# Kernel optimization log

Measured on AMD Instinct MI355X. Metric: run time of the kernel, lower is better.

## Reference

```python
import jax, jax.numpy as jnp
import numpy as np

DIM = 96; HEADS = 3; DHEAD = 32; GSS = 4; PATCH = 32; B = 128; G = 8
INNER = HEADS * DHEAD  # == DIM
SCALE = DHEAD ** -0.5
EPS = 1e-5


def _rbf(x):
    # FastKAN RBF basis on grid [-2, 2] with G centers -> (..., G)
    centers = jnp.linspace(-2.0, 2.0, G)
    h = 4.0 / (G - 1)
    return jnp.exp(-(((x[..., None] - centers) / h) ** 2))


def _kan_pointwise(x, wb, ws):
    # Pointwise KAN conv: (b, Cin, *spatial) -> (b, Cout, *spatial)
    # y = W_base @ silu(x) + W_spline @ rbf(x)
    b, cin = x.shape[0], x.shape[1]
    sp = x.shape[2:]
    xs = x.reshape(b, cin, -1)                       # (b, Cin, L)
    y = jnp.einsum('oi,bil->bol', wb, jax.nn.silu(xs))
    y = y + jnp.einsum('oig,bilg->bol', ws, _rbf(xs))
    return y.reshape(b, wb.shape[0], *sp)


def setup_inputs() -> dict:
    key = jax.random.key(0)
    ks = jax.random.split(key, 8)
    inp = {
        'x': jax.random.normal(ks[0], (B, DIM, PATCH, PATCH), jnp.float32),
        'group_tokens': jax.random.normal(ks[1], (DIM,), jnp.float32),
        'qkv_wb': jax.random.normal(ks[2], (3 * DIM, DIM), jnp.float32) * (DIM ** -0.5),
        'qkv_ws': jax.random.normal(ks[3], (3 * DIM, DIM, G), jnp.float32) * 0.02,
        'ln_g': jnp.ones((DHEAD,), jnp.float32),
        'ln_b': jnp.zeros((DHEAD,), jnp.float32),
        'gt_wb': jax.random.normal(ks[4], (2 * INNER, INNER), jnp.float32) * (INNER ** -0.5),
        'gt_ws': jax.random.normal(ks[5], (2 * INNER, INNER, G), jnp.float32) * 0.02,
        'out_wb': jax.random.normal(ks[6], (DIM, INNER), jnp.float32) * (INNER ** -0.5),
        'out_ws': jax.random.normal(ks[7], (DIM, INNER, G), jnp.float32) * 0.02,
    }
    return inp


def reference(x, group_tokens, qkv_wb, qkv_ws, ln_g, ln_b, gt_wb, gt_ws, out_wb, out_ws):
    b, c, H, W = x.shape
    g = GSS
    nx, ny = H // g, W // g
    nw = nx * ny                                    # number of windows
    bp = b * nw
    n = g * g + 1                                   # window tokens incl. group token

    # b c (h g1) (w g2) -> (b h w) c (g1 g2)
    xw = x.reshape(b, c, nx, g, ny, g).transpose(0, 2, 4, 1, 3, 5).reshape(bp, c, g * g)
    tok = jnp.broadcast_to(group_tokens[None, :, None], (bp, c, 1))
    xw = jnp.concatenate([tok, xw], axis=-1)        # (bp, c, n)

    qkv = _kan_pointwise(xw, qkv_wb, qkv_ws)        # (bp, 3c, n)
    q, k, v = jnp.split(qkv, 3, axis=1)

    def split_heads(t):  # b (h d) n -> b h n d
        return t.reshape(bp, HEADS, DHEAD, n).transpose(0, 1, 3, 2)

    q, k, v = map(split_heads, (q, k, v))
    q = q * SCALE
    # channel-attention within window: contract over token axis n
    dots = jnp.einsum('bhni,bhnj->bhij', q, k)      # (bp, h, d, d)
    attn = jax.nn.softmax(dots, axis=-1)
    out = jnp.einsum('bhij,bhnj->bhni', attn, v)    # (bp, h, n, d)

    gt = out[:, :, 0]                               # (bp, h, d) group tokens
    gf = out[:, :, 1:]                              # (bp, h, g*g, d)
    gt = gt.reshape(b, nw, HEADS, DHEAD).transpose(0, 2, 1, 3)            # (b, h, nw, d)
    gf = gf.reshape(b, nw, HEADS, g * g, DHEAD).transpose(0, 2, 1, 3, 4)  # (b, h, nw, gg, d)

    # group_tokens_to_qk: LN(d) -> GELU -> KAN conv over nw (channels h*d -> 2*h*d)
    mu = gt.mean(-1, keepdims=True)
    var = ((gt - mu) ** 2).mean(-1, keepdims=True)
    h_ = (gt - mu) * jax.lax.rsqrt(var + EPS) * ln_g + ln_b
    h_ = jax.nn.gelu(h_, approximate=False)
    hh = h_.transpose(0, 1, 3, 2).reshape(b, HEADS * DHEAD, nw)           # b (h c) n
    qk = _kan_pointwise(hh, gt_wb, gt_ws)                                 # (b, 2*h*d, nw)
    qk = qk.reshape(b, HEADS, 2 * DHEAD, nw).transpose(0, 1, 3, 2)        # (b, h, nw, 2d)
    w_q, w_k = jnp.split(qk, 2, axis=-1)
    w_q = w_q * SCALE
    w_attn = jax.nn.softmax(jnp.einsum('bhid,bhjd->bhij', w_q, w_k), axis=-1)
    agg = jnp.einsum('bhij,bhjwd->bhiwd', w_attn, gf)                     # (b, h, nw, gg, d)

    # b h (x y) (g1 g2) d -> b (h d) (x g1) (y g2)
    fmap = agg.reshape(b, HEADS, nx, ny, g, g, DHEAD)
    fmap = fmap.transpose(0, 1, 6, 2, 4, 3, 5).reshape(b, HEADS * DHEAD, H, W)

    return _kan_pointwise(fmap, out_wb, out_ws)     # (b, dim, H, W)
```

## Files before the change

kernel.cpp:

```cpp
#include <hip/hip_runtime.h>
#include <cstddef>

#define SCALE 0.17677669529663687f
#define EPS 1e-5f

typedef __attribute__((ext_vector_type(8))) __bf16 bf16x8;
typedef __attribute__((ext_vector_type(16))) float f32x16;
typedef __attribute__((ext_vector_type(8))) unsigned short ushort8;

__device__ __forceinline__ unsigned short f2bf(float f) {
    unsigned u = __float_as_uint(f);
    return (unsigned short)((u + 0x7fffu + ((u >> 16) & 1u)) >> 16);
}
__device__ __forceinline__ float bf2f(unsigned short h) {
    return __uint_as_float(((unsigned)h) << 16);
}
__device__ __forceinline__ unsigned cvt_pk_bf16(float a, float b) {
    unsigned r;
    asm("v_cvt_pk_bf16_f32 %0, %1, %2" : "=v"(r) : "v"(a), "v"(b));
    return r;
}

#define MFMA32(a, b, c) __builtin_amdgcn_mfma_f32_32x32x16_bf16(a, b, c, 0, 0, 0)

#define GLD_LDS16(gsrc, ldst) \
    __builtin_amdgcn_global_load_lds((const __attribute__((address_space(1))) void*)(gsrc), \
                                     (__attribute__((address_space(3))) void*)(ldst), 16, 0, 0)

__global__ __launch_bounds__(256)
void prep_frag32(const float* __restrict__ wb, const float* __restrict__ ws,
                 unsigned short* __restrict__ Wf, int MTT)
{
    int idx = blockIdx.x * 256 + threadIdx.x;
    int total = 27 * MTT * 4 * 64;
    if (idx >= total) return;
    int lane = idx & 63;
    int t = idx >> 6;
    int hl = t & 1, kf = (t >> 1) & 1;
    int mt = (t >> 2) % MTT, s = (t >> 2) / MTT;
    int cg = s / 9, f = s - cg * 9;
    int m = mt * 32 + (lane & 31);
    int kg = lane >> 5;
    ushort8 v;
    #pragma unroll
    for (int j = 0; j < 8; ++j) {
        int c = cg * 32 + kf * 16 + kg * 8 + j;
        float w = (f == 0) ? wb[m * 96 + c] : ws[(m * 96 + c) * 8 + (f - 1)];
        unsigned short hi = f2bf(w);
        v[j] = hl ? f2bf(w - bf2f(hi)) : hi;
    }
    *reinterpret_cast<ushort8*>(Wf + (size_t)t * 512 + lane * 8) = v;
}

template<int MTT, int MODE>
__global__ __launch_bounds__(256, 4)
void kan_mfma(const float* __restrict__ xin, const float* __restrict__ token,
              const unsigned short* __restrict__ Wf, float* __restrict__ out)
{
    __shared__ __align__(16) char smem[40960];
    char* sA = smem;
    char* sB = smem + 24576;

    const int tid = threadIdx.x, lane = tid & 63, wid = tid >> 6;

    int n0, mb;
    if (MODE == 0) {
        int xcd = blockIdx.x & 7, idx = blockIdx.x >> 3;
        int nloc = idx / 3; mb = idx - nloc * 3;
        n0 = (xcd * 136 + nloc) * 128;
    } else if (MODE == 1) {
        int xcd = blockIdx.x & 7;
        n0 = (xcd * 128 + (blockIdx.x >> 3)) * 128; mb = 0;
    } else {
        mb = blockIdx.x & 1; n0 = (blockIdx.x >> 1) * 128;
    }

    auto issueA = [&](int s, int buf) {
        #pragma unroll
        for (int c0 = 0; c0 < 3; ++c0) {
            int c = wid + c0 * 4;
            const unsigned short* src = Wf + ((size_t)s * MTT * 4 + mb * 12 + c) * 512 + lane * 8;
            GLD_LDS16(src, sA + (buf * 12 + c) * 1024);
        }
    };
    issueA(0, 0);

    const int ct = tid & 127, kgp = tid >> 7;
    const int lane_in = kgp * 32 + (ct & 31);
    const int p = n0 + ct;
    const float* gbase;
    int gstride;
    if (MODE == 0) {
        int w = p / 17, l = p - w * 17;
        if (l == 0) { gbase = token; gstride = 1; }
        else {
            int b = w >> 6, wl = w & 63;
            int wx = wl >> 3, wy = wl & 7;
            int jj = l - 1, gx = jj >> 2, gy = jj & 3;
            gbase = xin + (size_t)b * 98304 + (wx * 4 + gx) * 32 + wy * 4 + gy;
            gstride = 1024;
        }
    } else if (MODE == 1) {
        gbase = xin + (size_t)(p >> 10) * 98304 + (p & 1023);
        gstride = 1024;
    } else {
        gbase = xin + (size_t)(p >> 6) * 6144 + (p & 63);
        gstride = 64;
    }

    f32x16 acc[3];
    #pragma unroll
    for (int mt = 0; mt < 3; ++mt)
        #pragma unroll
        for (int r = 0; r < 16; ++r) acc[mt][r] = 0.f;

    float rr[16], du[16];

    auto phiInit = [&](int cg, char* d0, char* d1) {
        float ph[16];
        #pragma unroll
        for (int t = 0; t < 2; ++t)
            #pragma unroll
            for (int j = 0; j < 8; ++j) {
                int q = t * 8 + j;
                float xv = gbase[(size_t)(cg * 32 + t * 16 + kgp * 8 + j) * gstride];
                ph[q] = __fdividef(xv, 1.f + __expf(-xv));
                float a = fmaf(xv, 1.75f, 3.5f);
                rr[q] = __expf(-a * a);
                du[q] = __expf(fminf(fmaf(a, 2.f, -1.f), 80.f));
            }
        uint4 w0, w1;
        w0.x = cvt_pk_bf16(ph[0], ph[1]);  w0.y = cvt_pk_bf16(ph[2], ph[3]);
        w0.z = cvt_pk_bf16(ph[4], ph[5]);  w0.w = cvt_pk_bf16(ph[6], ph[7]);
        w1.x = cvt_pk_bf16(ph[8], ph[9]);  w1.y = cvt_pk_bf16(ph[10], ph[11]);
        w1.z = cvt_pk_bf16(ph[12], ph[13]); w1.w = cvt_pk_bf16(ph[14], ph[15]);
        *reinterpret_cast<uint4*>(d0) = w0;
        *reinterpret_cast<uint4*>(d1) = w1;
    };
    auto phiRbf = [&](bool upd, char* d0, char* d1) {
        if (upd) {
            #pragma unroll
            for (int q = 0; q < 16; ++q) { rr[q] *= du[q]; du[q] *= 0.1353352832366127f; }
        }
        uint4 w0, w1;
        w0.x = cvt_pk_bf16(rr[0], rr[1]);  w0.y = cvt_pk_bf16(rr[2], rr[3]);
        w0.z = cvt_pk_bf16(rr[4], rr[5]);  w0.w = cvt_pk_bf16(rr[6], rr[7]);
        w1.x = cvt_pk_bf16(rr[8], rr[9]);  w1.y = cvt_pk_bf16(rr[10], rr[11]);
        w1.z = cvt_pk_bf16(rr[12], rr[13]); w1.w = cvt_pk_bf16(rr[14], rr[15]);
        *reinterpret_cast<uint4*>(d0) = w0;
        *reinterpret_cast<uint4*>(d1) = w1;
    };

    phiInit(0, sB + (ct >> 5) * 1024 + lane_in * 16,
               sB + (4 + (ct >> 5)) * 1024 + lane_in * 16);

    #pragma unroll
    for (int s = 0; s < 27; ++s) {
        int sb = s & 1;
        __syncthreads();
        if (s + 1 < 27) issueA(s + 1, (s + 1) & 1);
        {
            const char* Ab = sA + sb * 12288;
            const char* Bb = sB + sb * 8192;
            bf16x8 b0 = *reinterpret_cast<const bf16x8*>(Bb + wid * 1024 + lane * 16);
            bf16x8 b1 = *reinterpret_cast<const bf16x8*>(Bb + (4 + wid) * 1024 + lane * 16);
            #pragma unroll
            for (int mt = 0; mt < 3; ++mt) {
                const char* fb = Ab + mt * 4096 + lane * 16;
                bf16x8 a0 = *reinterpret_cast<const bf16x8*>(fb);
                bf16x8 a1 = *reinterpret_cast<const bf16x8*>(fb + 1024);
                bf16x8 a2 = *reinterpret_cast<const bf16x8*>(fb + 2048);
                bf16x8 a3 = *reinterpret_cast<const bf16x8*>(fb + 3072);
                acc[mt] = MFMA32(a0, b0, acc[mt]);
                acc[mt] = MFMA32(a1, b0, acc[mt]);
                acc[mt] = MFMA32(a2, b1, acc[mt]);
                acc[mt] = MFMA32(a3, b1, acc[mt]);
            }
        }
        if (s + 1 < 27) {
            char* d0 = sB + ((s + 1) & 1) * 8192 + (ct >> 5) * 1024 + lane_in * 16;
            int fn = (s + 1) % 9;
            if (fn == 0) phiInit((s + 1) / 9, d0, d0 + 4096);
            else phiRbf(fn != 1, d0, d0 + 4096);
        }
    }

    if (MODE == 0) {
        float* T = reinterpret_cast<float*>(smem);
        const int cw = wid * 32 + (lane & 31);
        const int c2 = tid & 127, q = tid >> 7;
        const int pp = n0 + c2, w = pp / 17, l = pp - w * 17;
        float* dst = out + (size_t)w * 4896 + l * 288 + mb * 96 + q * 16;
        #pragma unroll
        for (int mt = 0; mt < 3; ++mt) {
            __syncthreads();
            #pragma unroll
            for (int r = 0; r < 16; ++r) {
                int row = (r & 3) + 8 * (r >> 2) + 4 * (lane >> 5);
                T[cw * 33 + row] = acc[mt][r];
            }
            __syncthreads();
            const float* srcT = T + c2 * 33 + q * 16;
            #pragma unroll
            for (int jj = 0; jj < 4; ++jj) {
                float4 v;
                v.x = srcT[jj * 4 + 0]; v.y = srcT[jj * 4 + 1];
                v.z = srcT[jj * 4 + 2]; v.w = srcT[jj * 4 + 3];
                reinterpret_cast<float4*>(dst + mt * 32)[jj] = v;
            }
        }
    } else {
        const int colL = n0 + wid * 32 + (lane & 31);
        #pragma unroll
        for (int mt = 0; mt < 3; ++mt) {
            #pragma unroll
            for (int r = 0; r < 16; ++r) {
                int row = mb * 96 + mt * 32 + (r & 3) + 8 * (r >> 2) + 4 * (lane >> 5);
                float v = acc[mt][r];
                if (MODE == 1)
                    out[(size_t)(colL >> 10) * 98304 + (size_t)row * 1024 + (colL & 1023)] = v;
                else
                    out[(size_t)row * 8192 + colL] = v;
            }
        }
    }
}

__global__ __launch_bounds__(256)
void attn1(const float* __restrict__ qkv, float* __restrict__ gt, float* __restrict__ gf)
{
    __shared__ float sw[17][288];
    __shared__ float sa[3][32][33];
    const int w = blockIdx.x, tid = threadIdx.x;

    const float4* src = reinterpret_cast<const float4*>(qkv + (size_t)w * 4896);
    float4* dstl = reinterpret_cast<float4*>(&sw[0][0]);
    for (int e = tid; e < 1224; e += 256) dstl[e] = src[e];
    __syncthreads();

    for (int e = tid; e < 3072; e += 256) {
        int h = e >> 10, r = e & 1023, i = r >> 5, j = r & 31;
        float s = 0.f;
        #pragma unroll
        for (int l = 0; l < 17; ++l) s += sw[l][h * 32 + i] * sw[l][96 + h * 32 + j];
        sa[h][i][j] = s * SCALE;
    }
    __syncthreads();
    if (tid < 96) {
        int h = tid >> 5, i = tid & 31;
        float m = -1e30f;
        for (int j = 0; j < 32; ++j) m = fmaxf(m, sa[h][i][j]);
        float sum = 0.f;
        for (int j = 0; j < 32; ++j) { float e_ = __expf(sa[h][i][j] - m); sa[h][i][j] = e_; sum += e_; }
        float inv = 1.f / sum;
        for (int j = 0; j < 32; ++j) sa[h][i][j] *= inv;
    }
    __syncthreads();
    const int b = w >> 6, wl = w & 63;
    for (int e = tid; e < 1632; e += 256) {
        int h = e / 544, r = e - h * 544, l = r >> 5, i = r & 31;
        float s = 0.f;
        #pragma unroll
        for (int j = 0; j < 32; ++j) s += sa[h][i][j] * sw[l][192 + h * 32 + j];
        if (l == 0) gt[(((size_t)b * 3 + h) * 64 + wl) * 32 + i] = s;
        else        gf[((((size_t)b * 3 + h) * 64 + wl) * 16 + (l - 1)) * 32 + i] = s;
    }
}

__global__ __launch_bounds__(256)
void ln_gelu(const float* __restrict__ gt, const float* __restrict__ lng,
             const float* __restrict__ lnb, float* __restrict__ hh)
{
    int row = blockIdx.x * 8 + (threadIdx.x >> 5);
    int d = threadIdx.x & 31;
    float x = gt[(size_t)row * 32 + d];
    float s = x, s2 = x * x;
    #pragma unroll
    for (int m = 16; m >= 1; m >>= 1) { s += __shfl_xor(s, m, 32); s2 += __shfl_xor(s2, m, 32); }
    float mu = s * (1.f / 32.f);
    float var = s2 * (1.f / 32.f) - mu * mu;
    float h = (x - mu) * rsqrtf(var + EPS) * lng[d] + lnb[d];
    float g = 0.5f * h * (1.f + erff(h * 0.70710678118654752f));
    int b = row / 192, r = row - b * 192;
    int hd = r >> 6, wl = r & 63;
    hh[((size_t)b * 96 + hd * 32 + d) * 64 + wl] = g;
}

__global__ __launch_bounds__(256)
void attn2a(const float* __restrict__ qk, float* __restrict__ wattn)
{
    int bh = blockIdx.x;
    int b = bh / 3, h = bh - b * 3;
    __shared__ float swq[64][33];
    __shared__ float swk[64][33];
    __shared__ float sd[64][65];
    int tid = threadIdx.x;
    for (int e = tid; e < 2048; e += 256) {
        int d = e >> 6, i = e & 63;
        swq[i][d] = qk[((size_t)h * 64 + d) * 8192 + b * 64 + i] * SCALE;
        swk[i][d] = qk[((size_t)h * 64 + 32 + d) * 8192 + b * 64 + i];
    }
    __syncthreads();
    for (int e = tid; e < 4096; e += 256) {
        int i = e >> 6, j = e & 63;
        float s = 0.f;
        #pragma unroll
        for (int d = 0; d < 32; ++d) s += swq[i][d] * swk[j][d];
        sd[i][j] = s;
    }
    __syncthreads();
    if (tid < 64) {
        float m = -1e30f;
        for (int j = 0; j < 64; ++j) m = fmaxf(m, sd[tid][j]);
        float sum = 0.f;
        for (int j = 0; j < 64; ++j) { float e_ = __expf(sd[tid][j] - m); sd[tid][j] = e_; sum += e_; }
        float inv = 1.f / sum;
        for (int j = 0; j < 64; ++j) sd[tid][j] *= inv;
    }
    __syncthreads();
    for (int e = tid; e < 4096; e += 256)
        wattn[(size_t)bh * 4096 + e] = sd[e >> 6][e & 63];
}

__global__ __launch_bounds__(256)
void attn2b(const float* __restrict__ wattn, const float* __restrict__ gf,
            float* __restrict__ fmap)
{
    int blk = blockIdx.x;
    int ct = blk & 3, bh = blk >> 2;
    int b = bh / 3, h = bh - b * 3;
    __shared__ float sa[64][65];
    __shared__ float sg[64][129];
    int tid = threadIdx.x;
    for (int e = tid; e < 4096; e += 256) sa[e >> 6][e & 63] = wattn[(size_t)bh * 4096 + e];
    for (int e = tid; e < 8192; e += 256) {
        int j = e >> 7, c = e & 127;
        sg[j][c] = gf[((size_t)bh * 64 + j) * 512 + ct * 128 + c];
    }
    __syncthreads();
    int txc = tid & 31, tyi = tid >> 5;
    float acc[8][4];
    #pragma unroll
    for (int ii = 0; ii < 8; ++ii)
        #pragma unroll
        for (int c = 0; c < 4; ++c) acc[ii][c] = 0.f;
    for (int j = 0; j < 64; ++j) {
        float g0[4];
        #pragma unroll
        for (int c = 0; c < 4; ++c) g0[c] = sg[j][txc + c * 32];
        #pragma unroll
        for (int ii = 0; ii < 8; ++ii) {
            float a = sa[tyi + ii * 8][j];
            #pragma unroll
            for (int c = 0; c < 4; ++c) acc[ii][c] += a * g0[c];
        }
    }
    __syncthreads();
    #pragma unroll
    for (int ii = 0; ii < 8; ++ii)
        #pragma unroll
        for (int c = 0; c < 4; ++c)
            sg[tyi + ii * 8][txc + c * 32] = acc[ii][c];
    __syncthreads();
    for (int e = tid; e < 8192; e += 256) {
        int d = e >> 8;
        int nx = (e >> 5) & 7;
        int cp = e & 31;
        int ny = cp >> 2, gy = cp & 3;
        float v = sg[nx * 8 + ny][gy * 32 + d];
        fmap[(((size_t)b * 96 + h * 32 + d) * 32 + nx * 4 + ct) * 32 + cp] = v;
    }
}

extern "C" void kernel_launch(void* const* d_in, const int* in_sizes, int n_in,
                              void* d_out, int out_size, void* d_ws, size_t ws_size,
                              hipStream_t stream)
{
    const float* x      = (const float*)d_in[0];
    const float* tok    = (const float*)d_in[1];
    const float* qkv_wb = (const float*)d_in[2];
    const float* qkv_ws = (const float*)d_in[3];
    const float* lng    = (const float*)d_in[4];
    const float* lnb    = (const float*)d_in[5];
    const float* gt_wb  = (const float*)d_in[6];
    const float* gt_ws  = (const float*)d_in[7];
    const float* out_wb = (const float*)d_in[8];
    const float* out_ws = (const float*)d_in[9];
    float* out = (float*)d_out;
    float* ws  = (float*)d_ws;

    const size_t OFF_QKV   = 0;
    const size_t OFF_FMAP  = 0;
    const size_t OFF_WATTN = 12582912;
    const size_t OFF_WF2   = 40108032;
    const size_t OFF_GT    = OFF_WF2 + 165888;
    const size_t OFF_GF    = OFF_GT + 786432;
    const size_t OFF_HH    = OFF_GF + 12582912;
    const size_t OFF_QK    = OFF_HH + 786432;
    const size_t OFF_WF1   = OFF_QK + 1572864;
    const size_t OFF_WF3   = OFF_WF1 + 248832;
    const size_t TOTAL     = OFF_WF3 + 82944;
    if (ws_size < TOTAL * sizeof(float)) return;

    unsigned short* wf1 = (unsigned short*)(ws + OFF_WF1);
    unsigned short* wf2 = (unsigned short*)(ws + OFF_WF2);
    unsigned short* wf3 = (unsigned short*)(ws + OFF_WF3);

    prep_frag32<<<243, 256, 0, stream>>>(qkv_wb, qkv_ws, wf1, 9);
    prep_frag32<<<162, 256, 0, stream>>>(gt_wb,  gt_ws,  wf2, 6);
    prep_frag32<<< 81, 256, 0, stream>>>(out_wb, out_ws, wf3, 3);

    kan_mfma<9, 0><<<3264, 256, 0, stream>>>(x, tok, wf1, ws + OFF_QKV);
    attn1<<<8192, 256, 0, stream>>>(ws + OFF_QKV, ws + OFF_GT, ws + OFF_GF);
    ln_gelu<<<3072, 256, 0, stream>>>(ws + OFF_GT, lng, lnb, ws + OFF_HH);
    kan_mfma<6, 2><<<128, 256, 0, stream>>>(ws + OFF_HH, nullptr, wf2, ws + OFF_QK);
    attn2a<<<384, 256, 0, stream>>>(ws + OFF_QK, ws + OFF_WATTN);
    attn2b<<<1536, 256, 0, stream>>>(ws + OFF_WATTN, ws + OFF_GF, ws + OFF_FMAP);
    kan_mfma<3, 1><<<1024, 256, 0, stream>>>(ws + OFF_FMAP, nullptr, wf3, out);
}
```

Measured before the change: 446.5 us.

## Keep activation fragments in registers and double the KAN GEMM N-tile

Restructures the KAN MFMA kernel so the activation basis values (silu and RBF) stay in registers as MFMA operands instead of being staged through shared memory. Each wave now covers 64 columns, so one block handles 256 points and the grid shrinks by half. The operand roles are swapped, which changes the accumulator layout: the QKV and QK outputs are now written directly in point-major order without an LDS transpose, and attn2a is changed to read QK in the new layout. This removes the shared-memory B traffic and barriers tied to it, at the cost of twice the accumulator registers, lower occupancy (launch bounds 2) and less coalesced direct stores.

```diff
diff --git a/kernel.cpp b/kernel.cpp
--- a/kernel.cpp
+++ b/kernel.cpp
@@ -53,26 +53,25 @@
 }
 
 template<int MTT, int MODE>
-__global__ __launch_bounds__(256, 4)
+__global__ __launch_bounds__(256, 2)
 void kan_mfma(const float* __restrict__ xin, const float* __restrict__ token,
               const unsigned short* __restrict__ Wf, float* __restrict__ out)
 {
-    __shared__ __align__(16) char smem[40960];
-    char* sA = smem;
-    char* sB = smem + 24576;
+    __shared__ __align__(16) char smem[2 * 12 * 1024];
 
     const int tid = threadIdx.x, lane = tid & 63, wid = tid >> 6;
+    const int kg = lane >> 5, cl = lane & 31;
 
     int n0, mb;
     if (MODE == 0) {
         int xcd = blockIdx.x & 7, idx = blockIdx.x >> 3;
         int nloc = idx / 3; mb = idx - nloc * 3;
-        n0 = (xcd * 136 + nloc) * 128;
+        n0 = (xcd * 68 + nloc) * 256;
     } else if (MODE == 1) {
         int xcd = blockIdx.x & 7;
-        n0 = (xcd * 128 + (blockIdx.x >> 3)) * 128; mb = 0;
+        n0 = (xcd * 64 + (blockIdx.x >> 3)) * 256; mb = 0;
     } else {
-        mb = blockIdx.x & 1; n0 = (blockIdx.x >> 1) * 128;
+        mb = blockIdx.x & 1; n0 = (blockIdx.x >> 1) * 256;
     }
 
     auto issueA = [&](int s, int buf) {
@@ -80,149 +79,170 @@
         for (int c0 = 0; c0 < 3; ++c0) {
             int c = wid + c0 * 4;
             const unsigned short* src = Wf + ((size_t)s * MTT * 4 + mb * 12 + c) * 512 + lane * 8;
-            GLD_LDS16(src, sA + (buf * 12 + c) * 1024);
+            GLD_LDS16(src, smem + (buf * 12 + c) * 1024);
         }
     };
     issueA(0, 0);
 
-    const int ct = tid & 127, kgp = tid >> 7;
-    const int lane_in = kgp * 32 + (ct & 31);
-    const int p = n0 + ct;
-    const float* gbase;
-    int gstride;
-    if (MODE == 0) {
-        int w = p / 17, l = p - w * 17;
-        if (l == 0) { gbase = token; gstride = 1; }
-        else {
-            int b = w >> 6, wl = w & 63;
-            int wx = wl >> 3, wy = wl & 7;
-            int jj = l - 1, gx = jj >> 2, gy = jj & 3;
-            gbase = xin + (size_t)b * 98304 + (wx * 4 + gx) * 32 + wy * 4 + gy;
-            gstride = 1024;
-        }
-    } else if (MODE == 1) {
-        gbase = xin + (size_t)(p >> 10) * 98304 + (p & 1023);
-        gstride = 1024;
-    } else {
-        gbase = xin + (size_t)(p >> 6) * 6144 + (p & 63);
-        gstride = 64;
-    }
-
-    f32x16 acc[3];
-    #pragma unroll
-    for (int mt = 0; mt < 3; ++mt)
-        #pragma unroll
-        for (int r = 0; r < 16; ++r) acc[mt][r] = 0.f;
-
-    float rr[16], du[16];
-
-    auto phiInit = [&](int cg, char* d0, char* d1) {
-        float ph[16];
-        #pragma unroll
-        for (int t = 0; t < 2; ++t)
-            #pragma unroll
-            for (int j = 0; j < 8; ++j) {
-                int q = t * 8 + j;
-                float xv = gbase[(size_t)(cg * 32 + t * 16 + kgp * 8 + j) * gstride];
-                ph[q] = __fdividef(xv, 1.f + __expf(-xv));
-                float a = fmaf(xv, 1.75f, 3.5f);
-                rr[q] = __expf(-a * a);
-                du[q] = __expf(fminf(fmaf(a, 2.f, -1.f), 80.f));
-            }
-        uint4 w0, w1;
-        w0.x = cvt_pk_bf16(ph[0], ph[1]);  w0.y = cvt_pk_bf16(ph[2], ph[3]);
-        w0.z = cvt_pk_bf16(ph[4], ph[5]);  w0.w = cvt_pk_bf16(ph[6], ph[7]);
-        w1.x = cvt_pk_bf16(ph[8], ph[9]);  w1.y = cvt_pk_bf16(ph[10], ph[11]);
-        w1.z = cvt_pk_bf16(ph[12], ph[13]); w1.w = cvt_pk_bf16(ph[14], ph[15]);
-        *reinterpret_cast<uint4*>(d0) = w0;
-        *reinterpret_cast<uint4*>(d1) = w1;
+    const float* gbv[2];
+    int gsv[2];
+    #pragma unroll
+    for (int nt = 0; nt < 2; ++nt) {
+        int p = n0 + wid * 64 + nt * 32 + cl;
+        if (MODE == 0) {
+            int w = p / 17, l = p - w * 17;
+            if (l == 0) { gbv[nt] = token; gsv[nt] = 1; }
+            else {
+                int b = w >> 6, wl = w & 63;
+                int wx = wl >> 3, wy = wl & 7;
+                int jj = l - 1, gx = jj >> 2, gy = jj & 3;
+                gbv[nt] = xin + (size_t)b * 98304 + (wx * 4 + gx) * 32 + wy * 4 + gy;
+                gsv[nt] = 1024;
+            }
+        } else if (MODE == 1) {
+            gbv[nt] = xin + (size_t)(p >> 10) * 98304 + (p & 1023);
+            gsv[nt] = 1024;
+        } else {
+            gbv[nt] = xin + (size_t)(p >> 6) * 6144 + (p & 63);
+            gsv[nt] = 64;
+        }
+    }
+
+    f32x16 acc[2][3];
+    #pragma unroll
+    for (int nt = 0; nt < 2; ++nt)
+        #pragma unroll
+        for (int mt = 0; mt < 3; ++mt)
+            #pragma unroll
+            for (int r = 0; r < 16; ++r) acc[nt][mt][r] = 0.f;
+
+    float rr[2][16], du[2][16];
+    bf16x8 pk[2][2];
+
+    auto phiInit = [&](int cg) {
+        #pragma unroll
+        for (int nt = 0; nt < 2; ++nt) {
+            float ph[16];
+            #pragma unroll
+            for (int t = 0; t < 2; ++t)
+                #pragma unroll
+                for (int j = 0; j < 8; ++j) {
+                    int q = t * 8 + j;
+                    float xv = gbv[nt][(size_t)(cg * 32 + t * 16 + kg * 8 + j) * gsv[nt]];
+                    ph[q] = __fdividef(xv, 1.f + __expf(-xv));
+                    float a = fmaf(xv, 1.75f, 3.5f);
+                    rr[nt][q] = __expf(-a * a);
+                    du[nt][q] = __expf(fminf(fmaf(a, 2.f, -1.f), 80.f));
+                }
+            #pragma unroll
+            for (int t = 0; t < 2; ++t) {
+                uint4 w;
+                w.x = cvt_pk_bf16(ph[t * 8 + 0], ph[t * 8 + 1]);
+                w.y = cvt_pk_bf16(ph[t * 8 + 2], ph[t * 8 + 3]);
+                w.z = cvt_pk_bf16(ph[t * 8 + 4], ph[t * 8 + 5]);
+                w.w = cvt_pk_bf16(ph[t * 8 + 6], ph[t * 8 + 7]);
+                pk[nt][t] = *reinterpret_cast<bf16x8*>(&w);
+            }
+        }
     };
-    auto phiRbf = [&](bool upd, char* d0, char* d1) {
-        if (upd) {
-            #pragma unroll
-            for (int q = 0; q < 16; ++q) { rr[q] *= du[q]; du[q] *= 0.1353352832366127f; }
-        }
-        uint4 w0, w1;
-        w0.x = cvt_pk_bf16(rr[0], rr[1]);  w0.y = cvt_pk_bf16(rr[2], rr[3]);
-        w0.z = cvt_pk_bf16(rr[4], rr[5]);  w0.w = cvt_pk_bf16(rr[6], rr[7]);
-        w1.x = cvt_pk_bf16(rr[8], rr[9]);  w1.y = cvt_pk_bf16(rr[10], rr[11]);
-        w1.z = cvt_pk_bf16(rr[12], rr[13]); w1.w = cvt_pk_bf16(rr[14], rr[15]);
-        *reinterpret_cast<uint4*>(d0) = w0;
-        *reinterpret_cast<uint4*>(d1) = w1;
+    auto phiRbf = [&](bool upd) {
+        #pragma unroll
+        for (int nt = 0; nt < 2; ++nt) {
+            if (upd) {
+                #pragma unroll
+                for (int q = 0; q < 16; ++q) { rr[nt][q] *= du[nt][q]; du[nt][q] *= 0.1353352832366127f; }
+            }
+            #pragma unroll
+            for (int t = 0; t < 2; ++t) {
+                uint4 w;
+                w.x = cvt_pk_bf16(rr[nt][t * 8 + 0], rr[nt][t * 8 + 1]);
+                w.y = cvt_pk_bf16(rr[nt][t * 8 + 2], rr[nt][t * 8 + 3]);
+                w.z = cvt_pk_bf16(rr[nt][t * 8 + 4], rr[nt][t * 8 + 5]);
+                w.w = cvt_pk_bf16(rr[nt][t * 8 + 6], rr[nt][t * 8 + 7]);
+                pk[nt][t] = *reinterpret_cast<bf16x8*>(&w);
+            }
+        }
     };
 
-    phiInit(0, sB + (ct >> 5) * 1024 + lane_in * 16,
-               sB + (4 + (ct >> 5)) * 1024 + lane_in * 16);
-
     #pragma unroll
     for (int s = 0; s < 27; ++s) {
-        int sb = s & 1;
         __syncthreads();
         if (s + 1 < 27) issueA(s + 1, (s + 1) & 1);
-        {
-            const char* Ab = sA + sb * 12288;
-            const char* Bb = sB + sb * 8192;
-            bf16x8 b0 = *reinterpret_cast<const bf16x8*>(Bb + wid * 1024 + lane * 16);
-            bf16x8 b1 = *reinterpret_cast<const bf16x8*>(Bb + (4 + wid) * 1024 + lane * 16);
-            #pragma unroll
-            for (int mt = 0; mt < 3; ++mt) {
-                const char* fb = Ab + mt * 4096 + lane * 16;
-                bf16x8 a0 = *reinterpret_cast<const bf16x8*>(fb);
-                bf16x8 a1 = *reinterpret_cast<const bf16x8*>(fb + 1024);
-                bf16x8 a2 = *reinterpret_cast<const bf16x8*>(fb + 2048);
-                bf16x8 a3 = *reinterpret_cast<const bf16x8*>(fb + 3072);
-                acc[mt] = MFMA32(a0, b0, acc[mt]);
-                acc[mt] = MFMA32(a1, b0, acc[mt]);
-                acc[mt] = MFMA32(a2, b1, acc[mt]);
-                acc[mt] = MFMA32(a3, b1, acc[mt]);
-            }
-        }
-        if (s + 1 < 27) {
-            char* d0 = sB + ((s + 1) & 1) * 8192 + (ct >> 5) * 1024 + lane_in * 16;
-            int fn = (s + 1) % 9;
-            if (fn == 0) phiInit((s + 1) / 9, d0, d0 + 4096);
-            else phiRbf(fn != 1, d0, d0 + 4096);
+        const int fn = s % 9;
+        if (fn == 0) phiInit(s / 9);
+        else phiRbf(fn != 1);
+
+        const char* Ab = smem + (s & 1) * 12288;
+        #pragma unroll
+        for (int mt = 0; mt < 3; ++mt) {
+            const char* fb = Ab + mt * 4096 + lane * 16;
+            bf16x8 b0h = *reinterpret_cast<const bf16x8*>(fb);
+            bf16x8 b0l = *reinterpret_cast<const bf16x8*>(fb + 1024);
+            bf16x8 b1h = *reinterpret_cast<const bf16x8*>(fb + 2048);
+            bf16x8 b1l = *reinterpret_cast<const bf16x8*>(fb + 3072);
+            #pragma unroll
+            for (int nt = 0; nt < 2; ++nt) {
+                acc[nt][mt] = MFMA32(pk[nt][0], b0h, acc[nt][mt]);
+                acc[nt][mt] = MFMA32(pk[nt][0], b0l, acc[nt][mt]);
+                acc[nt][mt] = MFMA32(pk[nt][1], b1h, acc[nt][mt]);
+                acc[nt][mt] = MFMA32(pk[nt][1], b1l, acc[nt][mt]);
+            }
         }
     }
 
     if (MODE == 0) {
+        #pragma unroll
+        for (int nt = 0; nt < 2; ++nt)
+            #pragma unroll
+            for (int r = 0; r < 16; ++r) {
+                int p = n0 + wid * 64 + nt * 32 + (r & 3) + 8 * (r >> 2) + 4 * kg;
+                int w = p / 17, l = p - w * 17;
+                float* dst = out + (size_t)w * 4896 + l * 288 + mb * 96 + cl;
+                dst[0]  = acc[nt][0][r];
+                dst[32] = acc[nt][1][r];
+                dst[64] = acc[nt][2][r];
+            }
+    } else if (MODE == 2) {
+        #pragma unroll
+        for (int nt = 0; nt < 2; ++nt)
+            #pragma unroll
+            for (int r = 0; r < 16; ++r) {
+                int p = n0 + wid * 64 + nt * 32 + (r & 3) + 8 * (r >> 2) + 4 * kg;
+                float* dst = out + (size_t)p * 192 + mb * 96 + cl;
+                dst[0]  = acc[nt][0][r];
+                dst[32] = acc[nt][1][r];
+                dst[64] = acc[nt][2][r];
+            }
+    } else {
         float* T = reinterpret_cast<float*>(smem);
-        const int cw = wid * 32 + (lane & 31);
-        const int c2 = tid & 127, q = tid >> 7;
-        const int pp = n0 + c2, w = pp / 17, l = pp - w * 17;
-        float* dst = out + (size_t)w * 4896 + l * 288 + mb * 96 + q * 16;
-        #pragma unroll
-        for (int mt = 0; mt < 3; ++mt) {
-            __syncthreads();
-            #pragma unroll
-            for (int r = 0; r < 16; ++r) {
-                int row = (r & 3) + 8 * (r >> 2) + 4 * (lane >> 5);
-                T[cw * 33 + row] = acc[mt][r];
-            }
-            __syncthreads();
-            const float* srcT = T + c2 * 33 + q * 16;
-            #pragma unroll
-            for (int jj = 0; jj < 4; ++jj) {
-                float4 v;
-                v.x = srcT[jj * 4 + 0]; v.y = srcT[jj * 4 + 1];
-                v.z = srcT[jj * 4 + 2]; v.w = srcT[jj * 4 + 3];
-                reinterpret_cast<float4*>(dst + mt * 32)[jj] = v;
-            }
-        }
-    } else {
-        const int colL = n0 + wid * 32 + (lane & 31);
-        #pragma unroll
-        for (int mt = 0; mt < 3; ++mt) {
-            #pragma unroll
-            for (int r = 0; r < 16; ++r) {
-                int row = mb * 96 + mt * 32 + (r & 3) + 8 * (r >> 2) + 4 * (lane >> 5);
-                float v = acc[mt][r];
-                if (MODE == 1)
-                    out[(size_t)(colL >> 10) * 98304 + (size_t)row * 1024 + (colL & 1023)] = v;
-                else
-                    out[(size_t)row * 8192 + colL] = v;
-            }
-        }
+        #pragma unroll
+        for (int mt = 0; mt < 3; ++mt)
+            #pragma unroll
+            for (int ch = 0; ch < 2; ++ch) {
+                __syncthreads();
+                if ((wid >> 1) == ch) {
+                    #pragma unroll
+                    for (int nt = 0; nt < 2; ++nt)
+                        #pragma unroll
+                        for (int r = 0; r < 16; ++r) {
+                            int pl = (wid & 1) * 64 + nt * 32 + (r & 3) + 8 * (r >> 2) + 4 * kg;
+                            T[cl * 129 + pl] = acc[nt][mt][r];
+                        }
+                }
+                __syncthreads();
+                int m = tid >> 3, p0 = (tid & 7) * 16;
+                int col = n0 + ch * 128 + p0;
+                const float* rowT = T + m * 129 + p0;
+                float* dst = out + (size_t)(col >> 10) * 98304
+                           + (size_t)(mb * 96 + mt * 32 + m) * 1024 + (col & 1023);
+                #pragma unroll
+                for (int j = 0; j < 16; j += 4) {
+                    float4 v;
+                    v.x = rowT[j + 0]; v.y = rowT[j + 1];
+                    v.z = rowT[j + 2]; v.w = rowT[j + 3];
+                    *reinterpret_cast<float4*>(dst + j) = v;
+                }
+            }
     }
 }
 
@@ -296,9 +316,10 @@
     __shared__ float sd[64][65];
     int tid = threadIdx.x;
     for (int e = tid; e < 2048; e += 256) {
-        int d = e >> 6, i = e & 63;
-        swq[i][d] = qk[((size_t)h * 64 + d) * 8192 + b * 64 + i] * SCALE;
-        swk[i][d] = qk[((size_t)h * 64 + 32 + d) * 8192 + b * 64 + i];
+        int i = e >> 5, d = e & 31;
+        const float* row = qk + ((size_t)b * 64 + i) * 192 + h * 64;
+        swq[i][d] = row[d] * SCALE;
+        swk[i][d] = row[32 + d];
     }
     __syncthreads();
     for (int e = tid; e < 4096; e += 256) {
@@ -410,11 +431,11 @@
     prep_frag32<<<162, 256, 0, stream>>>(gt_wb,  gt_ws,  wf2, 6);
     prep_frag32<<< 81, 256, 0, stream>>>(out_wb, out_ws, wf3, 3);
 
-    kan_mfma<9, 0><<<3264, 256, 0, stream>>>(x, tok, wf1, ws + OFF_QKV);
+    kan_mfma<9, 0><<<1632, 256, 0, stream>>>(x, tok, wf1, ws + OFF_QKV);
     attn1<<<8192, 256, 0, stream>>>(ws + OFF_QKV, ws + OFF_GT, ws + OFF_GF);
     ln_gelu<<<3072, 256, 0, stream>>>(ws + OFF_GT, lng, lnb, ws + OFF_HH);
-    kan_mfma<6, 2><<<128, 256, 0, stream>>>(ws + OFF_HH, nullptr, wf2, ws + OFF_QK);
+    kan_mfma<6, 2><<<64, 256, 0, stream>>>(ws + OFF_HH, nullptr, wf2, ws + OFF_QK);
     attn2a<<<384, 256, 0, stream>>>(ws + OFF_QK, ws + OFF_WATTN);
     attn2b<<<1536, 256, 0, stream>>>(ws + OFF_WATTN, ws + OFF_GF, ws + OFF_FMAP);
-    kan_mfma<3, 1><<<1024, 256, 0, stream>>>(ws + OFF_FMAP, nullptr, wf3, out);
-}
+    kan_mfma<3, 1><<<512, 256, 0, stream>>>(ws + OFF_FMAP, nullptr, wf3, out);
+}
```

Result: no change. 454.8 us (+1.9%).
